# Optimization experiments

Hardware: AMD Instinct MI355X
Metric: run time of the kernel (lower is better)

## Reference

```python
import jax, jax.numpy as jnp
import numpy as np

N, D = 1024, 256


def setup_inputs() -> dict:
    key = jax.random.key(0)
    k1, k2 = jax.random.split(key)
    mu_X = jax.random.normal(k1, (N, D), dtype=jnp.float32)
    log_sigma = jax.random.normal(k2, (N, D), dtype=jnp.float32)
    return {"mu_X": mu_X, "log_sigma": log_sigma}


def reference(mu_X, log_sigma):
    # F.normalize: x / max(||x||_2, eps), eps=1e-12
    norm = jnp.linalg.norm(mu_X, axis=-1, keepdims=True)
    mu = mu_X / jnp.maximum(norm, 1e-12)
    sigma_sq = jnp.exp(log_sigma)                       # [N, D]
    sig_sum = sigma_sq[:, None, :] + sigma_sq[None, :, :]  # [N, N, D]
    # pairwise squared diff weighted by summed variances + log-variance penalty
    diff = (mu[:, None, :] - mu[None, :, :]) ** 2 / (1e-10 + sig_sum) + jnp.log(sig_sum)
    return -diff.sum(axis=2)                            # [N, N]
```

## Files before the change

### kernel.cpp

```cpp
#include <hip/hip_runtime.h>

#define N 1024
#define D 256

#define RI 8
#define LDW 260

__global__ __launch_bounds__(256) void prep3(
    const float* __restrict__ muX, const float* __restrict__ ls,
    float2* __restrict__ msT2) {
  const int i0 = blockIdx.x * RI;
  const int t = threadIdx.x;
  __shared__ float smu[RI][LDW];
  __shared__ float ssg[RI][LDW];
  __shared__ float sred[RI][32];
  __shared__ float rden[RI];
  const float4* mu4 = (const float4*)(muX + (size_t)i0 * D);
  const float4* ls4 = (const float4*)(ls + (size_t)i0 * D);
#pragma unroll
  for (int u = 0; u < 2; ++u) {
    const int idx = u * 256 + t;
    const int row = idx >> 6, c4 = idx & 63;
    const float4 v = mu4[idx];
    *(float4*)&smu[row][c4 * 4] = v;
    const float4 e = ls4[idx];
    float4 x;
    x.x = __expf(e.x) + 5e-11f; x.y = __expf(e.y) + 5e-11f;
    x.z = __expf(e.z) + 5e-11f; x.w = __expf(e.w) + 5e-11f;
    *(float4*)&ssg[row][c4 * 4] = x;
  }
  __syncthreads();
  {
    const int r = t >> 5, q = t & 31;
    float s = 0.f;
#pragma unroll
    for (int k = 0; k < 8; ++k) {
      const float v = smu[r][q + 32 * k];
      s = fmaf(v, v, s);
    }
    sred[r][q] = s;
  }
  __syncthreads();
  if (t < RI) {
    float tot = 0.f;
    for (int u = 0; u < 32; ++u) tot += sred[t][u];
    rden[t] = 1.0f / fmaxf(sqrtf(tot), 1e-12f);
  }
  __syncthreads();
#pragma unroll
  for (int pass = 0; pass < 8; ++pass) {
    const int f = pass * 256 + t;
    const int b = f & 1, il = (f >> 1) & 7, g = f >> 4;
    const int d = 2 * g + b;
    msT2[((size_t)g * N + i0 + il) * 2 + b] =
        make_float2(smu[il][d] * rden[il], ssg[il][d]);
  }
}

__global__ __launch_bounds__(128) void pair_kernel(
    const float4* __restrict__ msT4, float* __restrict__ out) {
  int L = blockIdx.x;
  int js = 0, base = 0;
  while (L >= base + 64 * (js + 1)) { base += 64 * (js + 1); ++js; }
  const int ib = L - base;
  const int j0 = js * 128, i0 = ib * 2;
  const bool diag = (ib >= js * 64);
  const int j = j0 + threadIdx.x;

  float acc[2] = {0.f, 0.f};
  float p[2] = {1.f, 1.f};
  int ea[2] = {0, 0};

#pragma unroll 4
  for (int g = 0; g < D / 2; ++g) {
    const float4 jv = msT4[(size_t)g * N + j];
#pragma unroll
    for (int k = 0; k < 2; ++k) {
      const float4 iv = msT4[(size_t)g * N + i0 + k];
      {
        const float sv = iv.y + jv.y;
        const float t0 = iv.x - jv.x;
        acc[k] = fmaf(t0 * t0, __builtin_amdgcn_rcpf(sv), acc[k]);
        p[k] *= sv;
      }
      {
        const float sv = iv.w + jv.w;
        const float t0 = iv.z - jv.z;
        acc[k] = fmaf(t0 * t0, __builtin_amdgcn_rcpf(sv), acc[k]);
        p[k] *= sv;
      }
    }
    if (g & 1) {
#pragma unroll
      for (int k = 0; k < 2; ++k) {
        const int bb = __float_as_int(p[k]);
        ea[k] += bb >> 23;
        p[k] = __int_as_float((bb & 0x007fffff) | 0x3f800000);
      }
    }
  }

  constexpr float LN2 = 0.6931471805599453f;
  float v[2];
#pragma unroll
  for (int k = 0; k < 2; ++k) {
    const float lg2 = (float)(ea[k] - 127 * (D / 4)) + __log2f(p[k]);
    v[k] = -(acc[k] + LN2 * lg2);
  }

  if (!diag) {
    out[(size_t)i0 * N + j] = v[0];
    out[(size_t)(i0 + 1) * N + j] = v[1];
    *(float2*)(out + (size_t)j * N + i0) = make_float2(v[0], v[1]);
  } else {
#pragma unroll
    for (int k = 0; k < 2; ++k) {
      const int i = i0 + k;
      if (j >= i) out[(size_t)i * N + j] = v[k];
      if (j > i) out[(size_t)j * N + i] = v[k];
    }
  }
}

extern "C" void kernel_launch(void* const* d_in, const int* in_sizes, int n_in,
                              void* d_out, int out_size, void* d_ws, size_t ws_size,
                              hipStream_t stream) {
  const float* muX = (const float*)d_in[0];
  const float* ls  = (const float*)d_in[1];
  float* out = (float*)d_out;
  float2* msT2 = (float2*)d_ws;
  prep3<<<dim3(N / RI), dim3(256), 0, stream>>>(muX, ls, msT2);
  const int nblocks = 64 * (8 * 9 / 2);
  pair_kernel<<<dim3(nblocks), dim3(128), 0, stream>>>((const float4*)msT2,
                                                       out);
}
```

Baseline: 95.92 us.

## Use square 16x16 triangular tiles with LDS-transposed symmetric stores

Replaces the 2x128 row-strip tiling of the pairwise kernel with 16x16 square tiles over the upper triangle, indexing blocks by a closed-form triangular-number inverse. The mirrored (transposed) output is staged through a padded shared-memory tile so both the direct and the transposed writes are row-contiguous, replacing the old scattered float2 column writes. The cost is an extra barrier and LDS traffic per block. Each 16-wide j segment loads only 256 bytes per g step, which gives shorter coalesced reads from the workspace.

Result: slower. 109.3 us (+14.0%).

```diff
diff --git a/kernel.cpp b/kernel.cpp
--- a/kernel.cpp
+++ b/kernel.cpp
@@ -59,13 +59,23 @@
 
 __global__ __launch_bounds__(128) void pair_kernel(
     const float4* __restrict__ msT4, float* __restrict__ out) {
-  int L = blockIdx.x;
-  int js = 0, base = 0;
-  while (L >= base + 64 * (js + 1)) { base += 64 * (js + 1); ++js; }
-  const int ib = L - base;
-  const int j0 = js * 128, i0 = ib * 2;
-  const bool diag = (ib >= js * 64);
-  const int j = j0 + threadIdx.x;
+  const int l = blockIdx.x;
+  int b = (int)((sqrtf(8.f * (float)l + 1.f) - 1.f) * 0.5f);
+  while (b * (b + 1) / 2 > l) --b;
+  while ((b + 1) * (b + 2) / 2 <= l) ++b;
+  const int bi = l - b * (b + 1) / 2;
+  const int bj = b;
+  const int i0 = bi * 16, j0 = bj * 16;
+
+  const int t = threadIdx.x;
+  const int w = t >> 6;
+  const int lane = t & 63;
+  const int jj = lane & 15;
+  const int rr = lane >> 4;
+  const int r0 = w * 8 + rr * 2;
+
+  const float4* __restrict__ pj = msT4 + (j0 + jj);
+  const float4* __restrict__ pi = msT4 + (i0 + r0);
 
   float acc[2] = {0.f, 0.f};
   float p[2] = {1.f, 1.f};
@@ -73,10 +83,10 @@
 
 #pragma unroll 4
   for (int g = 0; g < D / 2; ++g) {
-    const float4 jv = msT4[(size_t)g * N + j];
+    const float4 jv = pj[(size_t)g * N];
 #pragma unroll
     for (int k = 0; k < 2; ++k) {
-      const float4 iv = msT4[(size_t)g * N + i0 + k];
+      const float4 iv = pi[(size_t)g * N + k];
       {
         const float sv = iv.y + jv.y;
         const float t0 = iv.x - jv.x;
@@ -108,16 +118,33 @@
     v[k] = -(acc[k] + LN2 * lg2);
   }
 
+  __shared__ float tile[16][17];
+  const bool diag = (bi == bj);
+
   if (!diag) {
-    out[(size_t)i0 * N + j] = v[0];
-    out[(size_t)(i0 + 1) * N + j] = v[1];
-    *(float2*)(out + (size_t)j * N + i0) = make_float2(v[0], v[1]);
+#pragma unroll
+    for (int k = 0; k < 2; ++k)
+      out[(size_t)(i0 + r0 + k) * N + (j0 + jj)] = v[k];
+#pragma unroll
+    for (int k = 0; k < 2; ++k) tile[r0 + k][jj] = v[k];
+    __syncthreads();
+#pragma unroll
+    for (int k = 0; k < 2; ++k) {
+      const int q = r0 + k;
+      out[(size_t)(j0 + q) * N + (i0 + jj)] = tile[jj][q];
+    }
   } else {
 #pragma unroll
     for (int k = 0; k < 2; ++k) {
-      const int i = i0 + k;
-      if (j >= i) out[(size_t)i * N + j] = v[k];
-      if (j > i) out[(size_t)j * N + i] = v[k];
+      const int r = r0 + k;
+      if (jj >= r) out[(size_t)(i0 + r) * N + (j0 + jj)] = v[k];
+      tile[r][jj] = v[k];
+    }
+    __syncthreads();
+#pragma unroll
+    for (int k = 0; k < 2; ++k) {
+      const int q = r0 + k;
+      if (q > jj) out[(size_t)(j0 + q) * N + (i0 + jj)] = tile[jj][q];
     }
   }
 }
@@ -130,7 +157,7 @@
   float* out = (float*)d_out;
   float2* msT2 = (float2*)d_ws;
   prep3<<<dim3(N / RI), dim3(256), 0, stream>>>(muX, ls, msT2);
-  const int nblocks = 64 * (8 * 9 / 2);
-  pair_kernel<<<dim3(nblocks), dim3(128), 0, stream>>>((const float4*)msT2,
-                                                       out);
+  const int ntiles = (N / 16) * (N / 16 + 1) / 2;
+  pair_kernel<<<dim3(ntiles), dim3(128), 0, stream>>>((const float4*)msT2,
+                                                      out);
 }
```

## Split feature dimension across two blocks and combine with atomic adds

Applied to the files above, without the earlier changes.

Splits the reduction over D into two halves, each handled by its own block, which doubles the grid. Partial sums go into the output with atomicAdd, and the output is zeroed first inside the prep kernel. The aim is more parallelism and occupancy, since the grid was only 2304 blocks of 128 threads. The cost is many more global atomic operations in place of plain and float2 stores, plus an extra zeroing write pass over the 4 MB output.

After: 132.1 us. 37.7% more time.

```diff
diff --git a/kernel.cpp b/kernel.cpp
--- a/kernel.cpp
+++ b/kernel.cpp
@@ -2,15 +2,20 @@
 
 #define N 1024
 #define D 256
+#define GH 64
 
 #define RI 8
 #define LDW 260
 
 __global__ __launch_bounds__(256) void prep3(
     const float* __restrict__ muX, const float* __restrict__ ls,
-    float2* __restrict__ msT2) {
+    float2* __restrict__ msT2, float4* __restrict__ out4) {
   const int i0 = blockIdx.x * RI;
   const int t = threadIdx.x;
+#pragma unroll
+  for (int u = 0; u < 8; ++u)
+    out4[(size_t)blockIdx.x * 2048 + u * 256 + t] =
+        make_float4(0.f, 0.f, 0.f, 0.f);
   __shared__ float smu[RI][LDW];
   __shared__ float ssg[RI][LDW];
   __shared__ float sred[RI][32];
@@ -60,6 +65,8 @@
 __global__ __launch_bounds__(128) void pair_kernel(
     const float4* __restrict__ msT4, float* __restrict__ out) {
   int L = blockIdx.x;
+  const int half = L & 1;
+  L >>= 1;
   int js = 0, base = 0;
   while (L >= base + 64 * (js + 1)) { base += 64 * (js + 1); ++js; }
   const int ib = L - base;
@@ -67,16 +74,18 @@
   const bool diag = (ib >= js * 64);
   const int j = j0 + threadIdx.x;
 
+  const float4* __restrict__ ph = msT4 + (size_t)(half * GH) * N;
+
   float acc[2] = {0.f, 0.f};
   float p[2] = {1.f, 1.f};
   int ea[2] = {0, 0};
 
 #pragma unroll 4
-  for (int g = 0; g < D / 2; ++g) {
-    const float4 jv = msT4[(size_t)g * N + j];
+  for (int gg = 0; gg < GH; ++gg) {
+    const float4 jv = ph[(size_t)gg * N + j];
 #pragma unroll
     for (int k = 0; k < 2; ++k) {
-      const float4 iv = msT4[(size_t)g * N + i0 + k];
+      const float4 iv = ph[(size_t)gg * N + i0 + k];
       {
         const float sv = iv.y + jv.y;
         const float t0 = iv.x - jv.x;
@@ -90,7 +99,7 @@
         p[k] *= sv;
       }
     }
-    if (g & 1) {
+    if (gg & 1) {
 #pragma unroll
       for (int k = 0; k < 2; ++k) {
         const int bb = __float_as_int(p[k]);
@@ -104,20 +113,21 @@
   float v[2];
 #pragma unroll
   for (int k = 0; k < 2; ++k) {
-    const float lg2 = (float)(ea[k] - 127 * (D / 4)) + __log2f(p[k]);
+    const float lg2 = (float)(ea[k] - 127 * (GH / 2)) + __log2f(p[k]);
     v[k] = -(acc[k] + LN2 * lg2);
   }
 
   if (!diag) {
-    out[(size_t)i0 * N + j] = v[0];
-    out[(size_t)(i0 + 1) * N + j] = v[1];
-    *(float2*)(out + (size_t)j * N + i0) = make_float2(v[0], v[1]);
+    atomicAdd(&out[(size_t)i0 * N + j], v[0]);
+    atomicAdd(&out[(size_t)(i0 + 1) * N + j], v[1]);
+    atomicAdd(&out[(size_t)j * N + i0], v[0]);
+    atomicAdd(&out[(size_t)j * N + i0 + 1], v[1]);
   } else {
 #pragma unroll
     for (int k = 0; k < 2; ++k) {
       const int i = i0 + k;
-      if (j >= i) out[(size_t)i * N + j] = v[k];
-      if (j > i) out[(size_t)j * N + i] = v[k];
+      if (j >= i) atomicAdd(&out[(size_t)i * N + j], v[k]);
+      if (j > i) atomicAdd(&out[(size_t)j * N + i], v[k]);
     }
   }
 }
@@ -129,8 +139,8 @@
   const float* ls  = (const float*)d_in[1];
   float* out = (float*)d_out;
   float2* msT2 = (float2*)d_ws;
-  prep3<<<dim3(N / RI), dim3(256), 0, stream>>>(muX, ls, msT2);
-  const int nblocks = 64 * (8 * 9 / 2);
+  prep3<<<dim3(N / RI), dim3(256), 0, stream>>>(muX, ls, msT2, (float4*)out);
+  const int nblocks = 2 * 64 * (8 * 9 / 2);
   pair_kernel<<<dim3(nblocks), dim3(128), 0, stream>>>((const float4*)msT2,
                                                        out);
 }
```

## Stage i-vectors in LDS and double-buffer j loads in registers

Applied to the files above, without the earlier changes.

The pair kernel now loads the two i-row vectors for all 128 groups into shared memory once per block, so the inner loop no longer issues repeated global loads for them. The j-column loads are software-pipelined with two 8-deep register buffers, so the next chunk is fetched while the current chunk is computed. This is meant to hide global memory latency. In exchange it raises register pressure and adds a block-wide barrier.

Measured after the change: 120.7 us. 1.26x slower.

```diff
diff --git a/kernel.cpp b/kernel.cpp
--- a/kernel.cpp
+++ b/kernel.cpp
@@ -57,6 +57,45 @@
   }
 }
 
+#define UPD(jv, iv, k)                                           \
+  {                                                              \
+    const float s0 = (iv).y + (jv).y;                            \
+    const float t0 = (iv).x - (jv).x;                            \
+    acc[k] = fmaf(t0 * t0, __builtin_amdgcn_rcpf(s0), acc[k]);   \
+    p[k] *= s0;                                                  \
+    const float s1 = (iv).w + (jv).w;                            \
+    const float t1 = (iv).z - (jv).z;                            \
+    acc[k] = fmaf(t1 * t1, __builtin_amdgcn_rcpf(s1), acc[k]);   \
+    p[k] *= s1;                                                  \
+  }
+
+#define STEP(jv, g, odd)                                         \
+  {                                                              \
+    const float4 iv0 = sI[2 * (g)];                              \
+    const float4 iv1 = sI[2 * (g) + 1];                          \
+    UPD(jv, iv0, 0)                                              \
+    UPD(jv, iv1, 1)                                              \
+    if (odd) {                                                   \
+      for (int k = 0; k < 2; ++k) {                              \
+        const int bb = __float_as_int(p[k]);                     \
+        ea[k] += bb >> 23;                                       \
+        p[k] = __int_as_float((bb & 0x007fffff) | 0x3f800000);   \
+      }                                                          \
+    }                                                            \
+  }
+
+#define CHUNK(r0, r1, r2, r3, r4, r5, r6, r7, g0)                \
+  STEP(r0, (g0) + 0, 0) STEP(r1, (g0) + 1, 1)                    \
+  STEP(r2, (g0) + 2, 0) STEP(r3, (g0) + 3, 1)                    \
+  STEP(r4, (g0) + 4, 0) STEP(r5, (g0) + 5, 1)                    \
+  STEP(r6, (g0) + 6, 0) STEP(r7, (g0) + 7, 1)
+
+#define LOADC(r0, r1, r2, r3, r4, r5, r6, r7, g0)                \
+  r0 = pj[(size_t)((g0) + 0) * N]; r1 = pj[(size_t)((g0) + 1) * N]; \
+  r2 = pj[(size_t)((g0) + 2) * N]; r3 = pj[(size_t)((g0) + 3) * N]; \
+  r4 = pj[(size_t)((g0) + 4) * N]; r5 = pj[(size_t)((g0) + 5) * N]; \
+  r6 = pj[(size_t)((g0) + 6) * N]; r7 = pj[(size_t)((g0) + 7) * N];
+
 __global__ __launch_bounds__(128) void pair_kernel(
     const float4* __restrict__ msT4, float* __restrict__ out) {
   int L = blockIdx.x;
@@ -67,37 +106,31 @@
   const bool diag = (ib >= js * 64);
   const int j = j0 + threadIdx.x;
 
+  __shared__ float4 sI[256];
+  {
+    const int t = threadIdx.x;
+    sI[2 * t] = msT4[(size_t)t * N + i0];
+    sI[2 * t + 1] = msT4[(size_t)t * N + i0 + 1];
+  }
+  __syncthreads();
+
+  const float4* __restrict__ pj = msT4 + j;
+
   float acc[2] = {0.f, 0.f};
   float p[2] = {1.f, 1.f};
   int ea[2] = {0, 0};
 
-#pragma unroll 4
-  for (int g = 0; g < D / 2; ++g) {
-    const float4 jv = msT4[(size_t)g * N + j];
-#pragma unroll
-    for (int k = 0; k < 2; ++k) {
-      const float4 iv = msT4[(size_t)g * N + i0 + k];
-      {
-        const float sv = iv.y + jv.y;
-        const float t0 = iv.x - jv.x;
-        acc[k] = fmaf(t0 * t0, __builtin_amdgcn_rcpf(sv), acc[k]);
-        p[k] *= sv;
-      }
-      {
-        const float sv = iv.w + jv.w;
-        const float t0 = iv.z - jv.z;
-        acc[k] = fmaf(t0 * t0, __builtin_amdgcn_rcpf(sv), acc[k]);
-        p[k] *= sv;
-      }
-    }
-    if (g & 1) {
-#pragma unroll
-      for (int k = 0; k < 2; ++k) {
-        const int bb = __float_as_int(p[k]);
-        ea[k] += bb >> 23;
-        p[k] = __int_as_float((bb & 0x007fffff) | 0x3f800000);
-      }
-    }
+  float4 a0, a1, a2, a3, a4, a5, a6, a7;
+  float4 b0, b1, b2, b3, b4, b5, b6, b7;
+  LOADC(a0, a1, a2, a3, a4, a5, a6, a7, 0)
+  LOADC(b0, b1, b2, b3, b4, b5, b6, b7, 8)
+
+  for (int c = 0; c < 16; c += 2) {
+    const int g0 = c * 8;
+    CHUNK(a0, a1, a2, a3, a4, a5, a6, a7, g0)
+    if (c + 2 < 16) { LOADC(a0, a1, a2, a3, a4, a5, a6, a7, g0 + 16) }
+    CHUNK(b0, b1, b2, b3, b4, b5, b6, b7, g0 + 8)
+    if (c + 3 < 16) { LOADC(b0, b1, b2, b3, b4, b5, b6, b7, g0 + 24) }
   }
 
   constexpr float LN2 = 0.6931471805599453f;
```
